# Kernel tuning notes

Measured on AMD Instinct MI355X. Metric: run time of the kernel, lower is better.

Reference implementation:

```python
import jax, jax.numpy as jnp
import numpy as np

B, N, DM, DE, H, L = 4, 256, 128, 8, 2 and 2, 8  # placeholder, real values below
B, N, DM, DE, H, L = 4, 256, 128, 8, 8, 2
D = DM // H  # per-head dim = 16
INNER = H * D


def setup_inputs() -> dict:
    key = jax.random.key(0)
    ks = jax.random.split(key, 20)
    nodes = jax.random.normal(ks[0], (B, N, DM), dtype=jnp.float32)
    edges = jax.random.normal(ks[1], (B, N, N, DE), dtype=jnp.float32)
    adjacency = (jax.random.uniform(ks[2], (B, N, N)) < 0.1).astype(jnp.float32)
    s = 0.02
    p = {
        'Wq': jax.random.normal(ks[3], (L, DM, INNER)) * s,
        'bq': jnp.zeros((L, INNER)),
        'Wk': jax.random.normal(ks[4], (L, DM, INNER)) * s,
        'bk': jnp.zeros((L, INNER)),
        'Wv': jax.random.normal(ks[5], (L, DM, INNER)) * s,
        'bv': jnp.zeros((L, INNER)),
        'We': jax.random.normal(ks[6], (L, DE, INNER)) * s,
        'be': jnp.zeros((L, INNER)),
        'Wres': jax.random.normal(ks[7], (L, DM, DM)) * s,
        'bres': jnp.zeros((L, DM)),
        'Wgate': jax.random.normal(ks[8], (L, 3 * DM, 1)) * s,
        'ln_g': jnp.ones((L, DM)),
        'ln_b': jnp.zeros((L, DM)),
    }
    return {'nodes': nodes, 'edges': edges, 'adjacency': adjacency, **p}


def _adj_softmax(sim, adj):
    # Faithful to source: torch.mean(x, dim, keepdim=True)[0] indexes batch 0,
    # giving a (N,1) shift broadcast over all batch*head rows.
    means = jnp.mean(sim, axis=-1, keepdims=True)[0]
    x_exp = jnp.exp(sim - means) * adj
    s = jnp.sum(x_exp, axis=-1, keepdims=True)
    s = jnp.where(s == 0, 1.0, s)
    return x_exp / s


def reference(nodes, edges, adjacency, Wq, bq, Wk, bk, Wv, bv, We, be,
              Wres, bres, Wgate, ln_g, ln_b):
    b, n, dm = nodes.shape
    h, d = H, DM // H
    scale = 1.0 / jnp.sqrt(jnp.float32(d))
    adj = jnp.broadcast_to(adjacency[:, None], (b, h, n, n)).reshape(b * h, n, n)
    x = nodes
    for l in range(L):  # fixed small layer count
        def heads(t):  # (b,n,h*d) -> (b*h, n, d)
            return t.reshape(b, n, h, d).transpose(0, 2, 1, 3).reshape(b * h, n, d)
        q = heads(x @ Wq[l] + bq[l])
        k = heads(x @ Wk[l] + bk[l])
        v = heads(x @ Wv[l] + bv[l])
        # edge features: (b,n,n,h,d) -> (b*h, n, n, d)
        e = (edges @ We[l] + be[l]).reshape(b, n, n, h, d)
        e = e.transpose(0, 3, 1, 2, 4).reshape(b * h, n, n, d)
        ke = k[:, None, :, :] + e
        ve = v[:, None, :, :] + e
        sim = jnp.einsum('bid,bijd->bij', q, ke) * scale
        attn = _adj_softmax(sim, adj)
        out = jnp.einsum('bij,bijd->bid', attn, ve)
        out = out.reshape(b, h, n, d).transpose(0, 2, 1, 3).reshape(b, n, h * d)
        # GatedResidual
        res = x @ Wres[l] + bres[l]
        gate_in = jnp.concatenate([out, res, out - res], axis=-1)
        g = jax.nn.sigmoid(gate_in @ Wgate[l])
        y = out * g + res * (1 - g)
        mu = jnp.mean(y, axis=-1, keepdims=True)
        var = jnp.var(y, axis=-1, keepdims=True)
        y = (y - mu) / jnp.sqrt(var + 1e-5) * ln_g[l] + ln_b[l]
        x = jax.nn.relu(y)
    return x
```

## Files before the change

kernel.cpp:

```cpp
#include <hip/hip_runtime.h>

#define BB 4
#define NN 256
#define DMM 128
#define DEE 8
#define HH 8
#define DD 16
#define LAYERS 2
#define SCALE 0.25f
#define PS 260
#define SS (BB*NN*DMM)

struct Params {
  const float *nodes, *edges, *adjacency;
  const float *Wq, *bq, *Wk, *bk, *Wv, *bv, *We, *be, *Wres, *bres, *Wgate, *lng, *lnb;
  const float *src;
  float *q, *k, *v, *res;
  float *out;
  int layer;
};

__global__ __launch_bounds__(256) void k_proj(Params P){
  const int t = threadIdx.x;
  const int m = t >> 6;
  const int cp = t & 63;
  const int row0 = blockIdx.x * 4;
  const int l = P.layer;
  const float *W, *bia; float* dst;
  if (m==0){ W = P.Wq + l*DMM*DMM; bia = P.bq + l*DMM; dst = P.q; }
  else if (m==1){ W = P.Wk + l*DMM*DMM; bia = P.bk + l*DMM; dst = P.k; }
  else if (m==2){ W = P.Wv + l*DMM*DMM; bia = P.bv + l*DMM; dst = P.v; }
  else { W = P.Wres + l*DMM*DMM; bia = P.bres + l*DMM; dst = P.res; }
  const float2 bv2 = *(const float2*)(bia + 2*cp);
  float acc0[4] = {bv2.x,bv2.x,bv2.x,bv2.x};
  float acc1[4] = {bv2.y,bv2.y,bv2.y,bv2.y};
  const float2* W2 = (const float2*)W;
  const float* xr = P.src + row0*DMM;
  #pragma unroll 8
  for (int kk=0; kk<DMM; kk++){
    float2 w = W2[kk*64+cp];
    #pragma unroll
    for (int r=0;r<4;r++){
      float xv = xr[r*DMM+kk];
      acc0[r] += xv*w.x; acc1[r] += xv*w.y;
    }
  }
  #pragma unroll
  for (int r=0;r<4;r++){
    *(float2*)(dst + (row0+r)*DMM + 2*cp) = make_float2(acc0[r], acc1[r]);
  }
}

__global__ __launch_bounds__(256) void k_mid(Params P){
  const int t = threadIdx.x;
  const int row0 = blockIdx.x*2;
  const int row1 = row0+1;
  const int b = row0 >> 8;

  __shared__ float xloc[2][128];
  __shared__ float qs[2][128];
  __shared__ float res_s[2][128];
  __shared__ float qwe_s[2][64];
  __shared__ float qbe_s[2][8];
  __shared__ float es[8*PS];
  __shared__ float ps[8*PS];
  __shared__ float red_s[32];
  __shared__ float ssum_s[8];
  __shared__ float g_s[64];
  __shared__ float red_a[2], red_b[2], red_c[2];

  if (t < 128){
    qs[0][t]    = P.q  [(size_t)row0*DMM + t];
    res_s[0][t] = P.res[(size_t)row0*DMM + t];
  } else {
    qs[1][t-128]    = P.q  [(size_t)row1*DMM + (t-128)];
    res_s[1][t-128] = P.res[(size_t)row1*DMM + (t-128)];
  }
  float ec[2][8]; float adjv[2];
  #pragma unroll
  for (int r=0;r<2;r++){
    const float4* er4 = (const float4*)(P.edges + ((size_t)(row0+r)*NN + t)*DEE);
    float4 e0 = er4[0], e1 = er4[1];
    ec[r][0]=e0.x; ec[r][1]=e0.y; ec[r][2]=e0.z; ec[r][3]=e0.w;
    ec[r][4]=e1.x; ec[r][5]=e1.y; ec[r][6]=e1.z; ec[r][7]=e1.w;
    adjv[r] = P.adjacency[(size_t)(row0+r)*NN + t];
  }
  __syncthreads();

  if (t < 128){
    const int r = t>>6, u = t&63, h = u>>3, c = u&7;
    const float* Wer = P.We + c*DMM + h*DD;
    float a = 0.f;
    #pragma unroll
    for (int d=0; d<DD; d++) a += qs[r][h*DD+d]*Wer[d];
    qwe_s[r][u] = a;
    if (c==0){
      const float* ber = P.be + h*DD;
      float a2=0.f;
      #pragma unroll
      for (int d=0; d<DD; d++) a2 += qs[r][h*DD+d]*ber[d];
      qbe_s[r][h] = a2;
    }
  }
  __syncthreads();

  for (int r=0; r<2; r++){
    {
      const int j = t;
      #pragma unroll
      for (int c=0;c<8;c++) es[c*PS+j] = ec[r][c];
      const float4* kr = (const float4*)(P.k + ((size_t)b*NN + j)*DMM);
      float preg[8];
      #pragma unroll
      for (int h=0; h<HH; h++){
        float4 k0=kr[h*4+0], k1=kr[h*4+1], k2=kr[h*4+2], k3=kr[h*4+3];
        const float4* q4 = (const float4*)(&qs[r][h*DD]);
        float4 qa=q4[0], qb=q4[1], qc=q4[2], qd=q4[3];
        float sim = qbe_s[r][h];
        sim += qa.x*k0.x + qa.y*k0.y + qa.z*k0.z + qa.w*k0.w;
        sim += qb.x*k1.x + qb.y*k1.y + qb.z*k1.z + qb.w*k1.w;
        sim += qc.x*k2.x + qc.y*k2.y + qc.z*k2.z + qc.w*k2.w;
        sim += qd.x*k3.x + qd.y*k3.y + qd.z*k3.z + qd.w*k3.w;
        const float4* qw4 = (const float4*)(&qwe_s[r][h*8]);
        float4 wA=qw4[0], wB=qw4[1];
        sim += ec[r][0]*wA.x + ec[r][1]*wA.y + ec[r][2]*wA.z + ec[r][3]*wA.w;
        sim += ec[r][4]*wB.x + ec[r][5]*wB.y + ec[r][6]*wB.z + ec[r][7]*wB.w;
        sim *= SCALE;
        float p = __expf(sim)*adjv[r];
        preg[h]=p; ps[h*PS+j]=p;
      }
      #pragma unroll
      for (int h=0; h<HH; h++){
        float v = preg[h];
        #pragma unroll
        for (int off=32; off; off>>=1) v += __shfl_xor(v, off, 64);
        if ((t&63)==0) red_s[(t>>6)*8+h] = v;
      }
    }
    __syncthreads();

    float pv = 0.f;
    if (t < 128){
      const int h = t>>4;
      const float* vcol = P.v + (size_t)b*NN*DMM + t;
      const float4* pr = (const float4*)(ps + h*PS);
      #pragma unroll 4
      for (int jq=0; jq<64; jq++){
        float4 pp = pr[jq];
        const float* vv = vcol + jq*4*DMM;
        pv += pp.x*vv[0] + pp.y*vv[DMM] + pp.z*vv[2*DMM] + pp.w*vv[3*DMM];
      }
    } else if (t < 192){
      const int h=(t-128)>>3, c=(t-128)&7;
      const float4* pr = (const float4*)(ps + h*PS);
      const float4* er = (const float4*)(es + c*PS);
      float g=0.f;
      #pragma unroll 4
      for (int jq=0; jq<64; jq++){
        float4 pp=pr[jq], ee=er[jq];
        g += pp.x*ee.x + pp.y*ee.y + pp.z*ee.z + pp.w*ee.w;
      }
      g_s[h*8+c]=g;
    } else if (t >= 248){
      const int h=t-248;
      ssum_s[h] = red_s[h]+red_s[8+h]+red_s[16+h]+red_s[24+h];
    }
    __syncthreads();

    float o=0.f, rr=0.f;
    if (t<128){
      const int h = t>>4;
      const float* Wec = P.We + t;
      float eacc=0.f;
      #pragma unroll
      for (int c=0;c<8;c++) eacc += Wec[c*DMM]*g_s[h*8+c];
      const float ssum = ssum_s[h];
      const float denom = (ssum==0.f)?1.f:ssum;
      const float bev = P.be[t];
      o = (pv + eacc + ssum*bev)/denom;
      rr = res_s[r][t];
      const float* Wg = P.Wgate;
      float contrib = o*Wg[t] + rr*Wg[DMM+t] + (o-rr)*Wg[2*DMM+t];
      #pragma unroll
      for (int off=32; off; off>>=1) contrib += __shfl_xor(contrib, off, 64);
      if ((t&63)==0) red_a[t>>6]=contrib;
    }
    __syncthreads();

    float y=0.f;
    if (t<128){
      const float gs = red_a[0]+red_a[1];
      const float gate = 1.f/(1.f+__expf(-gs));
      y = o*gate + rr*(1.f-gate);
      float s1=y, s2=y*y;
      #pragma unroll
      for (int off=32; off; off>>=1){ s1+=__shfl_xor(s1,off,64); s2+=__shfl_xor(s2,off,64); }
      if ((t&63)==0){ red_b[t>>6]=s1; red_c[t>>6]=s2; }
    }
    __syncthreads();

    if (t<128){
      const float mu  = (red_b[0]+red_b[1])*(1.f/128.f);
      const float var = (red_c[0]+red_c[1])*(1.f/128.f) - mu*mu;
      const float inv = rsqrtf(var+1e-5f);
      float yn = (y-mu)*inv*P.lng[t] + P.lnb[t];
      xloc[r][t] = fmaxf(yn, 0.f);
    }
    __syncthreads();
  }

  {
    const int m = t>>6, cp = t&63;
    const float *W, *bia; float* dst;
    if (m==0){ W=P.Wq+DMM*DMM;   bia=P.bq+DMM;   dst=P.q;   }
    else if (m==1){ W=P.Wk+DMM*DMM;   bia=P.bk+DMM;   dst=P.k;   }
    else if (m==2){ W=P.Wv+DMM*DMM;   bia=P.bv+DMM;   dst=P.v;   }
    else          { W=P.Wres+DMM*DMM; bia=P.bres+DMM; dst=P.res; }
    const float2 bv2 = *(const float2*)(bia+2*cp);
    float a00=bv2.x, a01=bv2.y, a10=bv2.x, a11=bv2.y;
    const float2* W2 = (const float2*)W;
    #pragma unroll 8
    for (int kk=0; kk<DMM; kk++){
      float2 w = W2[kk*64+cp];
      float x0 = xloc[0][kk], x1 = xloc[1][kk];
      a00 += x0*w.x; a01 += x0*w.y;
      a10 += x1*w.x; a11 += x1*w.y;
    }
    *(float2*)(dst + SS + (size_t)row0*DMM + 2*cp) = make_float2(a00,a01);
    *(float2*)(dst + SS + (size_t)row1*DMM + 2*cp) = make_float2(a10,a11);
  }
}

__global__ __launch_bounds__(256) void k_attn(Params P){
  const int t = threadIdx.x;
  const int b = blockIdx.x >> 8;
  const int i = blockIdx.x & 255;
  const int l = P.layer;

  __shared__ float qs[128];
  __shared__ float qwe_s[64];
  __shared__ float qbe_s[8];
  __shared__ float es[8*PS];
  __shared__ float ps[8*PS];
  __shared__ float red_s[32];
  __shared__ float ssum_s[8];
  __shared__ float g_s[64];
  __shared__ float res_s[128];
  __shared__ float red_a[2], red_b[2], red_c[2];

  if (t < 128) qs[t] = P.q[(b*NN+i)*DMM + t];
  __syncthreads();
  if (t < 64){
    const int h = t>>3, c = t&7;
    const float* Wer = P.We + l*DEE*DMM + c*DMM + h*DD;
    float a = 0.f;
    #pragma unroll
    for (int d=0; d<DD; d++) a += qs[h*DD+d]*Wer[d];
    qwe_s[t] = a;
    if (c==0){
      const float* ber = P.be + l*DMM + h*DD;
      float a2 = 0.f;
      #pragma unroll
      for (int d=0; d<DD; d++) a2 += qs[h*DD+d]*ber[d];
      qbe_s[h] = a2;
    }
  }
  __syncthreads();

  {
    const int j = t;
    const float4* er4 = (const float4*)(P.edges + ((size_t)(b*NN+i)*NN + j)*DEE);
    float4 e0 = er4[0], e1 = er4[1];
    float ec[8] = {e0.x,e0.y,e0.z,e0.w, e1.x,e1.y,e1.z,e1.w};
    #pragma unroll
    for (int c=0;c<8;c++) es[c*PS+j] = ec[c];
    const float adj = P.adjacency[(size_t)(b*NN+i)*NN + j];
    const float4* kr = (const float4*)(P.k + (b*NN+j)*DMM);
    const float* qg = P.q + (b*NN+i)*DMM;
    float preg[8];
    #pragma unroll
    for (int h=0; h<HH; h++){
      float4 k0 = kr[h*4+0], k1 = kr[h*4+1], k2 = kr[h*4+2], k3 = kr[h*4+3];
      const float* qh = qg + h*DD;
      float sim = qbe_s[h];
      sim += qh[0]*k0.x + qh[1]*k0.y + qh[2]*k0.z + qh[3]*k0.w;
      sim += qh[4]*k1.x + qh[5]*k1.y + qh[6]*k1.z + qh[7]*k1.w;
      sim += qh[8]*k2.x + qh[9]*k2.y + qh[10]*k2.z + qh[11]*k2.w;
      sim += qh[12]*k3.x + qh[13]*k3.y + qh[14]*k3.z + qh[15]*k3.w;
      const float4* qw4 = (const float4*)(qwe_s + h*8);
      float4 wA = qw4[0], wB = qw4[1];
      sim += ec[0]*wA.x + ec[1]*wA.y + ec[2]*wA.z + ec[3]*wA.w;
      sim += ec[4]*wB.x + ec[5]*wB.y + ec[6]*wB.z + ec[7]*wB.w;
      sim *= SCALE;
      float p = __expf(sim) * adj;
      preg[h] = p;
      ps[h*PS+j] = p;
    }
    #pragma unroll
    for (int h=0; h<HH; h++){
      float v = preg[h];
      #pragma unroll
      for (int off=32; off; off>>=1) v += __shfl_xor(v, off, 64);
      if ((t&63)==0) red_s[(t>>6)*8 + h] = v;
    }
  }
  __syncthreads();

  float pv = 0.f;
  if (t < 128){
    const int h = t>>4;
    const float* vcol = P.v + b*NN*DMM + t;
    const float4* pr = (const float4*)(ps + h*PS);
    #pragma unroll 4
    for (int jq=0; jq<64; jq++){
      float4 pp = pr[jq];
      const float* vv = vcol + jq*4*DMM;
      pv += pp.x*vv[0] + pp.y*vv[DMM] + pp.z*vv[2*DMM] + pp.w*vv[3*DMM];
    }
  } else if (t < 192){
    const int h = (t-128)>>3, c = (t-128)&7;
    const float4* pr = (const float4*)(ps + h*PS);
    const float4* er = (const float4*)(es + c*PS);
    float g = 0.f;
    #pragma unroll 4
    for (int jq=0; jq<64; jq++){
      float4 pp = pr[jq], ee = er[jq];
      g += pp.x*ee.x + pp.y*ee.y + pp.z*ee.z + pp.w*ee.w;
    }
    g_s[h*8+c] = g;
  } else {
    const int u = t - 192;
    const float2 rv = *(const float2*)(P.res + (b*NN+i)*DMM + 2*u);
    res_s[2*u] = rv.x; res_s[2*u+1] = rv.y;
    if (t >= 248){
      const int h = t - 248;
      ssum_s[h] = red_s[h] + red_s[8+h] + red_s[16+h] + red_s[24+h];
    }
  }
  __syncthreads();

  float o = 0.f, rr = 0.f;
  if (t < 128){
    const int h = t>>4;
    const float* Wec = P.We + l*DEE*DMM + t;
    float eacc = 0.f;
    #pragma unroll
    for (int c=0;c<8;c++) eacc += Wec[c*DMM] * g_s[h*8+c];
    const float ssum = ssum_s[h];
    const float denom = (ssum==0.f) ? 1.f : ssum;
    const float bev = P.be[l*DMM + t];
    o = (pv + eacc + ssum*bev) / denom;
    rr = res_s[t];
    const float* Wg = P.Wgate + l*3*DMM;
    float contrib = o*Wg[t] + rr*Wg[DMM+t] + (o-rr)*Wg[2*DMM+t];
    #pragma unroll
    for (int off=32; off; off>>=1) contrib += __shfl_xor(contrib, off, 64);
    if ((t&63)==0) red_a[t>>6] = contrib;
  }
  __syncthreads();

  float y = 0.f;
  if (t < 128){
    const float gs = red_a[0] + red_a[1];
    const float gate = 1.f/(1.f + __expf(-gs));
    y = o*gate + rr*(1.f-gate);
    float s1 = y, s2 = y*y;
    #pragma unroll
    for (int off=32; off; off>>=1){ s1 += __shfl_xor(s1, off, 64); s2 += __shfl_xor(s2, off, 64); }
    if ((t&63)==0){ red_b[t>>6] = s1; red_c[t>>6] = s2; }
  }
  __syncthreads();

  if (t < 128){
    const float mu  = (red_b[0]+red_b[1]) * (1.f/128.f);
    const float var = (red_c[0]+red_c[1]) * (1.f/128.f) - mu*mu;
    const float inv = rsqrtf(var + 1e-5f);
    float yn = (y - mu)*inv*P.lng[l*DMM+t] + P.lnb[l*DMM+t];
    yn = fmaxf(yn, 0.f);
    P.out[(b*NN+i)*DMM + t] = yn;
  }
}

extern "C" void kernel_launch(void* const* d_in, const int* in_sizes, int n_in,
                              void* d_out, int out_size, void* d_ws, size_t ws_size,
                              hipStream_t stream) {
  Params P;
  P.nodes     = (const float*)d_in[0];
  P.edges     = (const float*)d_in[1];
  P.adjacency = (const float*)d_in[2];
  P.Wq   = (const float*)d_in[3];  P.bq   = (const float*)d_in[4];
  P.Wk   = (const float*)d_in[5];  P.bk   = (const float*)d_in[6];
  P.Wv   = (const float*)d_in[7];  P.bv   = (const float*)d_in[8];
  P.We   = (const float*)d_in[9];  P.be   = (const float*)d_in[10];
  P.Wres = (const float*)d_in[11]; P.bres = (const float*)d_in[12];
  P.Wgate= (const float*)d_in[13];
  P.lng  = (const float*)d_in[14]; P.lnb  = (const float*)d_in[15];

  float* f = (float*)d_ws;
  float* qbuf = f;
  float* kbuf = f + 2*SS;
  float* vbuf = f + 4*SS;
  float* rbuf = f + 6*SS;
  P.out = (float*)d_out;

  P.layer = 0; P.src = P.nodes;
  P.q = qbuf; P.k = kbuf; P.v = vbuf; P.res = rbuf;
  hipLaunchKernelGGL(k_proj, dim3(256), dim3(256), 0, stream, P);

  hipLaunchKernelGGL(k_mid, dim3(BB*NN/2), dim3(256), 0, stream, P);

  P.layer = 1;
  P.q = qbuf + SS; P.k = kbuf + SS; P.v = vbuf + SS; P.res = rbuf + SS;
  hipLaunchKernelGGL(k_attn, dim3(BB*NN), dim3(256), 0, stream, P);
}
```

Baseline: 159.8 us.

## Process both rows concurrently in k_mid with 512 threads and halve k_proj rows

k_mid now launches 512 threads per block, one 256-thread half per row, so the two rows that were handled in a sequential loop are processed in parallel. Shared buffers are doubled for this, and the trailing layer-1 projection gives each wave a single row. k_proj handles 2 rows per block instead of 4, doubling its grid. The aim is more parallelism and fewer serial sync phases. The cost is double the shared memory per block, which may reduce occupancy, and less weight reuse per block in k_proj.

```diff
diff --git a/kernel.cpp b/kernel.cpp
--- a/kernel.cpp
+++ b/kernel.cpp
@@ -24,7 +24,7 @@
   const int t = threadIdx.x;
   const int m = t >> 6;
   const int cp = t & 63;
-  const int row0 = blockIdx.x * 4;
+  const int row0 = blockIdx.x * 2;
   const int l = P.layer;
   const float *W, *bia; float* dst;
   if (m==0){ W = P.Wq + l*DMM*DMM; bia = P.bq + l*DMM; dst = P.q; }
@@ -32,29 +32,26 @@
   else if (m==2){ W = P.Wv + l*DMM*DMM; bia = P.bv + l*DMM; dst = P.v; }
   else { W = P.Wres + l*DMM*DMM; bia = P.bres + l*DMM; dst = P.res; }
   const float2 bv2 = *(const float2*)(bia + 2*cp);
-  float acc0[4] = {bv2.x,bv2.x,bv2.x,bv2.x};
-  float acc1[4] = {bv2.y,bv2.y,bv2.y,bv2.y};
+  float a00=bv2.x, a01=bv2.y, a10=bv2.x, a11=bv2.y;
   const float2* W2 = (const float2*)W;
-  const float* xr = P.src + row0*DMM;
+  const float* xr = P.src + (size_t)row0*DMM;
   #pragma unroll 8
   for (int kk=0; kk<DMM; kk++){
     float2 w = W2[kk*64+cp];
-    #pragma unroll
-    for (int r=0;r<4;r++){
-      float xv = xr[r*DMM+kk];
-      acc0[r] += xv*w.x; acc1[r] += xv*w.y;
-    }
-  }
-  #pragma unroll
-  for (int r=0;r<4;r++){
-    *(float2*)(dst + (row0+r)*DMM + 2*cp) = make_float2(acc0[r], acc1[r]);
-  }
+    float x0 = xr[kk], x1 = xr[DMM+kk];
+    a00 += x0*w.x; a01 += x0*w.y;
+    a10 += x1*w.x; a11 += x1*w.y;
+  }
+  *(float2*)(dst + (size_t)row0*DMM     + 2*cp) = make_float2(a00,a01);
+  *(float2*)(dst + (size_t)(row0+1)*DMM + 2*cp) = make_float2(a10,a11);
 }
 
-__global__ __launch_bounds__(256) void k_mid(Params P){
+__global__ __launch_bounds__(512) void k_mid(Params P){
   const int t = threadIdx.x;
+  const int r = t >> 8;
+  const int u = t & 255;
   const int row0 = blockIdx.x*2;
-  const int row1 = row0+1;
+  const int row  = row0 + r;
   const int b = row0 >> 8;
 
   __shared__ float xloc[2][128];
@@ -62,33 +59,30 @@
   __shared__ float res_s[2][128];
   __shared__ float qwe_s[2][64];
   __shared__ float qbe_s[2][8];
-  __shared__ float es[8*PS];
-  __shared__ float ps[8*PS];
-  __shared__ float red_s[32];
-  __shared__ float ssum_s[8];
-  __shared__ float g_s[64];
-  __shared__ float red_a[2], red_b[2], red_c[2];
-
-  if (t < 128){
-    qs[0][t]    = P.q  [(size_t)row0*DMM + t];
-    res_s[0][t] = P.res[(size_t)row0*DMM + t];
-  } else {
-    qs[1][t-128]    = P.q  [(size_t)row1*DMM + (t-128)];
-    res_s[1][t-128] = P.res[(size_t)row1*DMM + (t-128)];
-  }
-  float ec[2][8]; float adjv[2];
-  #pragma unroll
-  for (int r=0;r<2;r++){
-    const float4* er4 = (const float4*)(P.edges + ((size_t)(row0+r)*NN + t)*DEE);
+  __shared__ float es[2][8*PS];
+  __shared__ float ps[2][8*PS];
+  __shared__ float red_s[2][32];
+  __shared__ float ssum_s[2][8];
+  __shared__ float g_s[2][64];
+  __shared__ float red_a[2][2], red_b[2][2], red_c[2][2];
+
+  if (u < 128) qs[r][u]        = P.q  [(size_t)row*DMM + u];
+  else         res_s[r][u-128] = P.res[(size_t)row*DMM + (u-128)];
+  const int j = u;
+  float ec[8]; float adj;
+  {
+    const float4* er4 = (const float4*)(P.edges + ((size_t)row*NN + j)*DEE);
     float4 e0 = er4[0], e1 = er4[1];
-    ec[r][0]=e0.x; ec[r][1]=e0.y; ec[r][2]=e0.z; ec[r][3]=e0.w;
-    ec[r][4]=e1.x; ec[r][5]=e1.y; ec[r][6]=e1.z; ec[r][7]=e1.w;
-    adjv[r] = P.adjacency[(size_t)(row0+r)*NN + t];
-  }
-  __syncthreads();
-
-  if (t < 128){
-    const int r = t>>6, u = t&63, h = u>>3, c = u&7;
+    ec[0]=e0.x; ec[1]=e0.y; ec[2]=e0.z; ec[3]=e0.w;
+    ec[4]=e1.x; ec[5]=e1.y; ec[6]=e1.z; ec[7]=e1.w;
+    #pragma unroll
+    for (int c=0;c<8;c++) es[r][c*PS+j] = ec[c];
+    adj = P.adjacency[(size_t)row*NN + j];
+  }
+  __syncthreads();
+
+  if (u < 64){
+    const int h = u>>3, c = u&7;
     const float* Wer = P.We + c*DMM + h*DD;
     float a = 0.f;
     #pragma unroll
@@ -104,130 +98,124 @@
   }
   __syncthreads();
 
-  for (int r=0; r<2; r++){
-    {
-      const int j = t;
+  {
+    const float4* kr = (const float4*)(P.k + ((size_t)b*NN + j)*DMM);
+    float preg[8];
+    #pragma unroll
+    for (int h=0; h<HH; h++){
+      float4 k0=kr[h*4+0], k1=kr[h*4+1], k2=kr[h*4+2], k3=kr[h*4+3];
+      const float4* q4 = (const float4*)(&qs[r][h*DD]);
+      float4 qa=q4[0], qb=q4[1], qc=q4[2], qd=q4[3];
+      float sim = qbe_s[r][h];
+      sim += qa.x*k0.x + qa.y*k0.y + qa.z*k0.z + qa.w*k0.w;
+      sim += qb.x*k1.x + qb.y*k1.y + qb.z*k1.z + qb.w*k1.w;
+      sim += qc.x*k2.x + qc.y*k2.y + qc.z*k2.z + qc.w*k2.w;
+      sim += qd.x*k3.x + qd.y*k3.y + qd.z*k3.z + qd.w*k3.w;
+      const float4* qw4 = (const float4*)(&qwe_s[r][h*8]);
+      float4 wA=qw4[0], wB=qw4[1];
+      sim += ec[0]*wA.x + ec[1]*wA.y + ec[2]*wA.z + ec[3]*wA.w;
+      sim += ec[4]*wB.x + ec[5]*wB.y + ec[6]*wB.z + ec[7]*wB.w;
+      sim *= SCALE;
+      float p = __expf(sim)*adj;
+      preg[h]=p; ps[r][h*PS+j]=p;
+    }
+    #pragma unroll
+    for (int h=0; h<HH; h++){
+      float v = preg[h];
       #pragma unroll
-      for (int c=0;c<8;c++) es[c*PS+j] = ec[r][c];
-      const float4* kr = (const float4*)(P.k + ((size_t)b*NN + j)*DMM);
-      float preg[8];
-      #pragma unroll
-      for (int h=0; h<HH; h++){
-        float4 k0=kr[h*4+0], k1=kr[h*4+1], k2=kr[h*4+2], k3=kr[h*4+3];
-        const float4* q4 = (const float4*)(&qs[r][h*DD]);
-        float4 qa=q4[0], qb=q4[1], qc=q4[2], qd=q4[3];
-        float sim = qbe_s[r][h];
-        sim += qa.x*k0.x + qa.y*k0.y + qa.z*k0.z + qa.w*k0.w;
-        sim += qb.x*k1.x + qb.y*k1.y + qb.z*k1.z + qb.w*k1.w;
-        sim += qc.x*k2.x + qc.y*k2.y + qc.z*k2.z + qc.w*k2.w;
-        sim += qd.x*k3.x + qd.y*k3.y + qd.z*k3.z + qd.w*k3.w;
-        const float4* qw4 = (const float4*)(&qwe_s[r][h*8]);
-        float4 wA=qw4[0], wB=qw4[1];
-        sim += ec[r][0]*wA.x + ec[r][1]*wA.y + ec[r][2]*wA.z + ec[r][3]*wA.w;
-        sim += ec[r][4]*wB.x + ec[r][5]*wB.y + ec[r][6]*wB.z + ec[r][7]*wB.w;
-        sim *= SCALE;
-        float p = __expf(sim)*adjv[r];
-        preg[h]=p; ps[h*PS+j]=p;
-      }
-      #pragma unroll
-      for (int h=0; h<HH; h++){
-        float v = preg[h];
-        #pragma unroll
-        for (int off=32; off; off>>=1) v += __shfl_xor(v, off, 64);
-        if ((t&63)==0) red_s[(t>>6)*8+h] = v;
-      }
-    }
-    __syncthreads();
-
-    float pv = 0.f;
-    if (t < 128){
-      const int h = t>>4;
-      const float* vcol = P.v + (size_t)b*NN*DMM + t;
-      const float4* pr = (const float4*)(ps + h*PS);
-      #pragma unroll 4
-      for (int jq=0; jq<64; jq++){
-        float4 pp = pr[jq];
-        const float* vv = vcol + jq*4*DMM;
-        pv += pp.x*vv[0] + pp.y*vv[DMM] + pp.z*vv[2*DMM] + pp.w*vv[3*DMM];
-      }
-    } else if (t < 192){
-      const int h=(t-128)>>3, c=(t-128)&7;
-      const float4* pr = (const float4*)(ps + h*PS);
-      const float4* er = (const float4*)(es + c*PS);
-      float g=0.f;
-      #pragma unroll 4
-      for (int jq=0; jq<64; jq++){
-        float4 pp=pr[jq], ee=er[jq];
-        g += pp.x*ee.x + pp.y*ee.y + pp.z*ee.z + pp.w*ee.w;
-      }
-      g_s[h*8+c]=g;
-    } else if (t >= 248){
-      const int h=t-248;
-      ssum_s[h] = red_s[h]+red_s[8+h]+red_s[16+h]+red_s[24+h];
-    }
-    __syncthreads();
-
-    float o=0.f, rr=0.f;
-    if (t<128){
-      const int h = t>>4;
-      const float* Wec = P.We + t;
-      float eacc=0.f;
-      #pragma unroll
-      for (int c=0;c<8;c++) eacc += Wec[c*DMM]*g_s[h*8+c];
-      const float ssum = ssum_s[h];
-      const float denom = (ssum==0.f)?1.f:ssum;
-      const float bev = P.be[t];
-      o = (pv + eacc + ssum*bev)/denom;
-      rr = res_s[r][t];
-      const float* Wg = P.Wgate;
-      float contrib = o*Wg[t] + rr*Wg[DMM+t] + (o-rr)*Wg[2*DMM+t];
-      #pragma unroll
-      for (int off=32; off; off>>=1) contrib += __shfl_xor(contrib, off, 64);
-      if ((t&63)==0) red_a[t>>6]=contrib;
-    }
-    __syncthreads();
-
-    float y=0.f;
-    if (t<128){
-      const float gs = red_a[0]+red_a[1];
-      const float gate = 1.f/(1.f+__expf(-gs));
-      y = o*gate + rr*(1.f-gate);
-      float s1=y, s2=y*y;
-      #pragma unroll
-      for (int off=32; off; off>>=1){ s1+=__shfl_xor(s1,off,64); s2+=__shfl_xor(s2,off,64); }
-      if ((t&63)==0){ red_b[t>>6]=s1; red_c[t>>6]=s2; }
-    }
-    __syncthreads();
-
-    if (t<128){
-      const float mu  = (red_b[0]+red_b[1])*(1.f/128.f);
-      const float var = (red_c[0]+red_c[1])*(1.f/128.f) - mu*mu;
-      const float inv = rsqrtf(var+1e-5f);
-      float yn = (y-mu)*inv*P.lng[t] + P.lnb[t];
-      xloc[r][t] = fmaxf(yn, 0.f);
-    }
-    __syncthreads();
-  }
+      for (int off=32; off; off>>=1) v += __shfl_xor(v, off, 64);
+      if ((u&63)==0) red_s[r][(u>>6)*8+h] = v;
+    }
+  }
+  __syncthreads();
+
+  float pv = 0.f;
+  if (u < 128){
+    const int h = u>>4;
+    const float* vcol = P.v + (size_t)b*NN*DMM + u;
+    const float4* pr = (const float4*)(&ps[r][h*PS]);
+    #pragma unroll 4
+    for (int jq=0; jq<64; jq++){
+      float4 pp = pr[jq];
+      const float* vv = vcol + jq*4*DMM;
+      pv += pp.x*vv[0] + pp.y*vv[DMM] + pp.z*vv[2*DMM] + pp.w*vv[3*DMM];
+    }
+  } else if (u < 192){
+    const int h=(u-128)>>3, c=(u-128)&7;
+    const float4* pr = (const float4*)(&ps[r][h*PS]);
+    const float4* er = (const float4*)(&es[r][c*PS]);
+    float g=0.f;
+    #pragma unroll 4
+    for (int jq=0; jq<64; jq++){
+      float4 pp=pr[jq], ee=er[jq];
+      g += pp.x*ee.x + pp.y*ee.y + pp.z*ee.z + pp.w*ee.w;
+    }
+    g_s[r][h*8+c]=g;
+  } else if (u >= 248){
+    const int h=u-248;
+    ssum_s[r][h] = red_s[r][h]+red_s[r][8+h]+red_s[r][16+h]+red_s[r][24+h];
+  }
+  __syncthreads();
+
+  float o=0.f, rr=0.f;
+  if (u<128){
+    const int h = u>>4;
+    const float* Wec = P.We + u;
+    float eacc=0.f;
+    #pragma unroll
+    for (int c=0;c<8;c++) eacc += Wec[c*DMM]*g_s[r][h*8+c];
+    const float ssum = ssum_s[r][h];
+    const float denom = (ssum==0.f)?1.f:ssum;
+    const float bev = P.be[u];
+    o = (pv + eacc + ssum*bev)/denom;
+    rr = res_s[r][u];
+    const float* Wg = P.Wgate;
+    float contrib = o*Wg[u] + rr*Wg[DMM+u] + (o-rr)*Wg[2*DMM+u];
+    #pragma unroll
+    for (int off=32; off; off>>=1) contrib += __shfl_xor(contrib, off, 64);
+    if ((u&63)==0) red_a[r][u>>6]=contrib;
+  }
+  __syncthreads();
+
+  float y=0.f;
+  if (u<128){
+    const float gs = red_a[r][0]+red_a[r][1];
+    const float gate = 1.f/(1.f+__expf(-gs));
+    y = o*gate + rr*(1.f-gate);
+    float s1=y, s2=y*y;
+    #pragma unroll
+    for (int off=32; off; off>>=1){ s1+=__shfl_xor(s1,off,64); s2+=__shfl_xor(s2,off,64); }
+    if ((u&63)==0){ red_b[r][u>>6]=s1; red_c[r][u>>6]=s2; }
+  }
+  __syncthreads();
+
+  if (u<128){
+    const float mu  = (red_b[r][0]+red_b[r][1])*(1.f/128.f);
+    const float var = (red_c[r][0]+red_c[r][1])*(1.f/128.f) - mu*mu;
+    const float inv = rsqrtf(var+1e-5f);
+    float yn = (y-mu)*inv*P.lng[u] + P.lnb[u];
+    xloc[r][u] = fmaxf(yn, 0.f);
+  }
+  __syncthreads();
 
   {
-    const int m = t>>6, cp = t&63;
+    const int w = t>>6, m = w&3, ri = w>>2, cp = t&63;
     const float *W, *bia; float* dst;
     if (m==0){ W=P.Wq+DMM*DMM;   bia=P.bq+DMM;   dst=P.q;   }
     else if (m==1){ W=P.Wk+DMM*DMM;   bia=P.bk+DMM;   dst=P.k;   }
     else if (m==2){ W=P.Wv+DMM*DMM;   bia=P.bv+DMM;   dst=P.v;   }
     else          { W=P.Wres+DMM*DMM; bia=P.bres+DMM; dst=P.res; }
     const float2 bv2 = *(const float2*)(bia+2*cp);
-    float a00=bv2.x, a01=bv2.y, a10=bv2.x, a11=bv2.y;
+    float a0=bv2.x, a1=bv2.y;
     const float2* W2 = (const float2*)W;
+    const float* xr = xloc[ri];
     #pragma unroll 8
     for (int kk=0; kk<DMM; kk++){
-      float2 w = W2[kk*64+cp];
-      float x0 = xloc[0][kk], x1 = xloc[1][kk];
-      a00 += x0*w.x; a01 += x0*w.y;
-      a10 += x1*w.x; a11 += x1*w.y;
-    }
-    *(float2*)(dst + SS + (size_t)row0*DMM + 2*cp) = make_float2(a00,a01);
-    *(float2*)(dst + SS + (size_t)row1*DMM + 2*cp) = make_float2(a10,a11);
+      float2 w2 = W2[kk*64+cp];
+      float xv = xr[kk];
+      a0 += xv*w2.x; a1 += xv*w2.y;
+    }
+    *(float2*)(dst + SS + (size_t)(row0+ri)*DMM + 2*cp) = make_float2(a0,a1);
   }
 }
 
@@ -405,9 +393,9 @@
 
   P.layer = 0; P.src = P.nodes;
   P.q = qbuf; P.k = kbuf; P.v = vbuf; P.res = rbuf;
-  hipLaunchKernelGGL(k_proj, dim3(256), dim3(256), 0, stream, P);
-
-  hipLaunchKernelGGL(k_mid, dim3(BB*NN/2), dim3(256), 0, stream, P);
+  hipLaunchKernelGGL(k_proj, dim3(BB*NN/2), dim3(256), 0, stream, P);
+
+  hipLaunchKernelGGL(k_mid, dim3(BB*NN/2), dim3(512), 0, stream, P);
 
   P.layer = 1;
   P.q = qbuf + SS; P.k = kbuf + SS; P.v = vbuf + SS; P.res = rbuf + SS;
```

Result: slower. 169.6 us (+6.2%).
